# Performance work log

Hardware: AMD Instinct MI355X
Metric: run time of the kernel (lower is better)

## Reference

```python
import jax, jax.numpy as jnp
import numpy as np

GRAD_WEIGHT = 0.1
EPS = 1e-08


def _relative_l2(pred, target, eps):
    b = pred.shape[0]
    pf = pred.reshape(b, -1)
    tf = target.reshape(b, -1)
    num = jnp.linalg.norm(pf - tf, axis=1)
    den = jnp.maximum(jnp.linalg.norm(tf, axis=1), eps)
    return jnp.mean(num / den)


def _knn_gradient_norm(field, pos, knn_indices, eps):
    # field: (B,T,N,C); pos: (B,N,3); knn_indices: (B,N,K)
    # neigh_pos[b,n,k,:] = pos[b, knn[b,n,k], :]
    neigh_pos = jax.vmap(lambda p, idx: p[idx])(pos, knn_indices)  # (B,N,K,3)
    rel_pos = neigh_pos - pos[:, :, None, :]
    dist_sq = jnp.maximum(jnp.sum(rel_pos * rel_pos, axis=-1), eps)  # (B,N,K)
    dist = jnp.maximum(jnp.sqrt(dist_sq), eps)
    # neigh_field[b,t,n,k,:] = field[b,t,knn[b,n,k],:]
    neigh_field = jax.vmap(lambda f, idx: f[:, idx, :])(field, knn_indices)  # (B,T,N,K,C)
    rel_field = neigh_field - field[:, :, :, None, :]
    grad_mag = jnp.abs(rel_field) / dist[:, None, :, :, None]
    return jnp.mean(grad_mag, axis=(1, 2, 3, 4))  # (B,)


def setup_inputs() -> dict:
    key = jax.random.key(0)
    k1, k2, k3, k4 = jax.random.split(key, 4)
    B, T, N, C, K = 4, 8, 16384, 4, 16
    pred = jax.random.normal(k1, (B, T, N, C), dtype=jnp.float32)
    target = jax.random.normal(k2, (B, T, N, C), dtype=jnp.float32)
    knn_indices = jax.random.randint(k3, (B, N, K), 0, N, dtype=jnp.int64)
    pos = jax.random.uniform(k4, (B, N, 3), dtype=jnp.float32)
    return {"pred": pred, "target": target, "knn_indices": knn_indices, "pos": pos}


def reference(pred, target, knn_indices, pos):
    rl2 = _relative_l2(pred, target, EPS)
    pred_grad = _knn_gradient_norm(pred, pos, knn_indices, EPS)
    target_grad = _knn_gradient_norm(target, pos, knn_indices, EPS)
    grad_error = jnp.mean(jnp.abs(pred_grad - target_grad) / jnp.maximum(target_grad, EPS))
    return rl2 + GRAD_WEIGHT * grad_error
```

## Files before the change

kernel.cpp:

```cpp
#include <hip/hip_runtime.h>
#include <hip/hip_fp8.h>

#define NB   4
#define NT   8
#define NPTS 16384
#define NK   16
#define GRAD_COUNT 8388608.0f

#define P_BYTES     (NB * NPTS * 64)
#define REC_OFF_B   P_BYTES
#define PARTA_OFF_B (P_BYTES + NB * NPTS * NK * 8)
#define PARTB_OFF_B (PARTA_OFF_B + 65536)
#define WS_NEEDED   (PARTB_OFF_B + 8192)

#define PACK_BLOCKS 1024
#define DIST_BLOCKS 4096
#define PREP_BLOCKS (PACK_BLOCKS + DIST_BLOCKS)

#if defined(__has_builtin)
#if __has_builtin(__builtin_amdgcn_cvt_pk_f32_fp8) && __has_builtin(__builtin_amdgcn_cvt_pk_fp8_f32)
#define USE_FP8_BUILTINS 1
#endif
#endif

typedef float vf2 __attribute__((ext_vector_type(2)));

__device__ __forceinline__ unsigned pack4_fp8(float a, float b, float c, float d) {
#ifdef USE_FP8_BUILTINS
    int u = __builtin_amdgcn_cvt_pk_fp8_f32(a, b, 0, false);
    u     = __builtin_amdgcn_cvt_pk_fp8_f32(c, d, u, true);
    return (unsigned)u;
#else
    __hip_fp8_e4m3 ha(a), hb(b), hc(c), hd(d);
    return (unsigned)ha.__x | ((unsigned)hb.__x << 8) |
           ((unsigned)hc.__x << 16) | ((unsigned)hd.__x << 24);
#endif
}

__device__ __forceinline__ float absdiff4(unsigned a, unsigned b) {
#ifdef USE_FP8_BUILTINS
    vf2 a0 = __builtin_amdgcn_cvt_pk_f32_fp8((int)a, false);
    vf2 a1 = __builtin_amdgcn_cvt_pk_f32_fp8((int)a, true);
    vf2 b0 = __builtin_amdgcn_cvt_pk_f32_fp8((int)b, false);
    vf2 b1 = __builtin_amdgcn_cvt_pk_f32_fp8((int)b, true);
    return fabsf(a0.x - b0.x) + fabsf(a0.y - b0.y) +
           fabsf(a1.x - b1.x) + fabsf(a1.y - b1.y);
#else
    float s = 0.f;
    #pragma unroll
    for (int i = 0; i < 4; ++i) {
        __hip_fp8_e4m3 ha, hb;
        ha.__x = (a >> (8 * i)) & 0xff;
        hb.__x = (b >> (8 * i)) & 0xff;
        s += fabsf((float)ha - (float)hb);
    }
    return s;
#endif
}


__global__ __launch_bounds__(256) void sobolev_prep(
    const float4* __restrict__ pred,
    const float4* __restrict__ target,
    const float*  __restrict__ pos,
    const int*    __restrict__ knn,
    uint4*  __restrict__ P,
    int2*   __restrict__ REC,
    float*  __restrict__ partB)
{
    __shared__ float lds[4][2];

    if (blockIdx.x < PACK_BLOCKS) {
        const int blk = blockIdx.x;
        const int b   = blk >> 8;
        const int n   = ((blk & 255) << 6) + (threadIdx.x >> 2);
        const int q   = threadIdx.x & 3;

        const float4 pv0 = pred  [(b * NT + q    ) * NPTS + n];
        const float4 pv1 = pred  [(b * NT + q + 4) * NPTS + n];
        const float4 tv0 = target[(b * NT + q    ) * NPTS + n];
        const float4 tv1 = target[(b * NT + q + 4) * NPTS + n];

        uint4 ck;
        ck.x = pack4_fp8(pv0.x, pv0.y, pv0.z, pv0.w);
        ck.y = pack4_fp8(pv1.x, pv1.y, pv1.z, pv1.w);
        ck.z = pack4_fp8(tv0.x, tv0.y, tv0.z, tv0.w);
        ck.w = pack4_fp8(tv1.x, tv1.y, tv1.z, tv1.w);
        P[((size_t)(b * NPTS + n) << 2) + q] = ck;

        float sd, st;
        {
            const float e0 = pv0.x - tv0.x, e1 = pv0.y - tv0.y,
                        e2 = pv0.z - tv0.z, e3 = pv0.w - tv0.w;
            const float f0 = pv1.x - tv1.x, f1 = pv1.y - tv1.y,
                        f2 = pv1.z - tv1.z, f3 = pv1.w - tv1.w;
            sd = e0*e0 + e1*e1 + e2*e2 + e3*e3 + f0*f0 + f1*f1 + f2*f2 + f3*f3;
            st = tv0.x*tv0.x + tv0.y*tv0.y + tv0.z*tv0.z + tv0.w*tv0.w +
                 tv1.x*tv1.x + tv1.y*tv1.y + tv1.z*tv1.z + tv1.w*tv1.w;
        }

        const int wave = threadIdx.x >> 6, lane = threadIdx.x & 63;
        #pragma unroll
        for (int o = 32; o > 0; o >>= 1) {
            sd += __shfl_down(sd, o);
            st += __shfl_down(st, o);
        }
        if (lane == 0) { lds[wave][0] = sd; lds[wave][1] = st; }
        __syncthreads();
        if (threadIdx.x < 2)
            partB[blk * 2 + threadIdx.x] =
                lds[0][threadIdx.x] + lds[1][threadIdx.x] +
                lds[2][threadIdx.x] + lds[3][threadIdx.x];
    } else {
        const int t  = (blockIdx.x - PACK_BLOCKS) * 256 + threadIdx.x;
        const int b  = t >> 18;
        const int nk = t & 262143;
        const int n  = nk >> 4;
        const int j  = knn[t];

        const float* pb_ = pos + (size_t)b * NPTS * 3;
        const float jx = pb_[j * 3], jy = pb_[j * 3 + 1], jz = pb_[j * 3 + 2];
        const float nx = pb_[n * 3], ny = pb_[n * 3 + 1], nz = pb_[n * 3 + 2];
        const float dx = jx - nx, dy = jy - ny, dz = jz - nz;
        const float d2 = fmaxf(dx*dx + dy*dy + dz*dz, 1e-8f);
        const float inv_d = rsqrtf(d2);

        REC[t] = make_int2(j, __float_as_int(inv_d));
    }
}


__global__ __launch_bounds__(256) void sobolev_grad(
    const uint4* __restrict__ P,
    const int2*  __restrict__ REC,
    float*       __restrict__ partA)
{
    const int xcd  = blockIdx.x & 7;
    const int b    = xcd >> 1;
    const int nblk = ((xcd & 1) << 10) | (blockIdx.x >> 3);
    const int wave = threadIdx.x >> 6;
    const int lane = threadIdx.x & 63;
    const int k    = lane >> 2;
    const int q    = lane & 3;
    const int n0   = (nblk << 3) | (wave << 1);
    const int n1   = n0 | 1;

    const int2 r0 = REC[(((b << 14) | n0) << 4) | k];
    const int2 r1 = REC[(((b << 14) | n1) << 4) | k];
    const int j0 = r0.x, j1 = r1.x;
    const float inv_d0 = __int_as_float(r0.y);
    const float inv_d1 = __int_as_float(r1.y);

    const size_t pb = (size_t)(b * NPTS);
    const uint4 gj0 = P[((pb + j0) << 2) + q];
    const uint4 gn0 = P[((pb + n0) << 2) + q];
    const uint4 gj1 = P[((pb + j1) << 2) + q];
    const uint4 gn1 = P[((pb + n1) << 2) + q];

    const float sp0 = absdiff4(gj0.x, gn0.x) + absdiff4(gj0.y, gn0.y);
    const float st0 = absdiff4(gj0.z, gn0.z) + absdiff4(gj0.w, gn0.w);
    const float sp1 = absdiff4(gj1.x, gn1.x) + absdiff4(gj1.y, gn1.y);
    const float st1 = absdiff4(gj1.z, gn1.z) + absdiff4(gj1.w, gn1.w);

    float v0 = sp0 * inv_d0 + sp1 * inv_d1;
    float v1 = st0 * inv_d0 + st1 * inv_d1;

    __shared__ float lds[4][2];
    #pragma unroll
    for (int o = 32; o > 0; o >>= 1) {
        v0 += __shfl_down(v0, o);
        v1 += __shfl_down(v1, o);
    }
    if (lane == 0) { lds[wave][0] = v0; lds[wave][1] = v1; }
    __syncthreads();
    if (threadIdx.x < 2) {
        const int slot = (b << 11) | nblk;
        partA[slot * 2 + threadIdx.x] =
            lds[0][threadIdx.x] + lds[1][threadIdx.x] +
            lds[2][threadIdx.x] + lds[3][threadIdx.x];
    }
}

__global__ __launch_bounds__(1024) void sobolev_final(
    const float* __restrict__ partA,
    const float* __restrict__ partB,
    float*       __restrict__ out)
{
    const int tid = threadIdx.x;
    __shared__ float acc[NB][4];
    __shared__ float red[16][4];

    for (int b = 0; b < NB; ++b) {
        float pg = 0.f, tg = 0.f, sd = 0.f, st = 0.f;
        {
            const float2 v0 = ((const float2*)(partA + b * 2048 * 2))[tid];
            pg += v0.x; tg += v0.y;
            const float2 v1 = ((const float2*)(partA + b * 2048 * 2))[tid + 1024];
            pg += v1.x; tg += v1.y;
        }
        if (tid < 256) {
            const float2 vb = ((const float2*)(partB + b * 256 * 2))[tid];
            sd = vb.x; st = vb.y;
        }
        #pragma unroll
        for (int o = 32; o > 0; o >>= 1) {
            pg += __shfl_down(pg, o); tg += __shfl_down(tg, o);
            sd += __shfl_down(sd, o); st += __shfl_down(st, o);
        }
        const int wave = tid >> 6, lane = tid & 63;
        if (lane == 0) {
            red[wave][0] = pg; red[wave][1] = tg;
            red[wave][2] = sd; red[wave][3] = st;
        }
        __syncthreads();
        if (tid < 4) {
            float s = 0.f;
            #pragma unroll
            for (int w = 0; w < 16; ++w) s += red[w][tid];
            acc[b][tid] = s;
        }
        __syncthreads();
    }

    if (tid == 0) {
        float rl2 = 0.f, ge = 0.f;
        const float inv_cnt = 1.0f / GRAD_COUNT;
        #pragma unroll
        for (int b = 0; b < NB; ++b) {
            const float pg = acc[b][0] * inv_cnt;
            const float tg = acc[b][1] * inv_cnt;
            rl2 += sqrtf(acc[b][2]) / fmaxf(sqrtf(acc[b][3]), 1e-8f);
            ge  += fabsf(pg - tg) / fmaxf(tg, 1e-8f);
        }
        out[0] = rl2 * 0.25f + 0.1f * (ge * 0.25f);
    }
}


__global__ __launch_bounds__(256) void sobolev_main_fb(
    const float4* __restrict__ pred,
    const float4* __restrict__ target,
    const int*    __restrict__ knn,
    const float*  __restrict__ pos,
    float*        __restrict__ part)
{
    const int xcd   = blockIdx.x & 7;
    const int s     = blockIdx.x >> 3;
    const int b     = xcd >> 1;
    const int thalf = xcd & 1;
    const int w     = s * 256 + threadIdx.x;
    const int k     = w & (NK - 1);
    const int n     = w >> 4;
    const int j     = knn[(b << 18) + w];

    const float* pc = pos + (b * NPTS + n) * 3;
    const float* pj = pos + (b * NPTS + j) * 3;
    const float dx = pj[0] - pc[0], dy = pj[1] - pc[1], dz = pj[2] - pc[2];
    const float d2   = fmaxf(dx*dx + dy*dy + dz*dz, 1e-8f);
    const float dist = fmaxf(sqrtf(d2), 1e-8f);
    const float inv_d = 1.0f / dist;

    float pg_abs = 0.f, tg_abs = 0.f, sd = 0.f, st = 0.f;
    const bool do_l2 = (k == 0);
    const int t0 = thalf * 4;
    #pragma unroll
    for (int tt = 0; tt < 4; ++tt) {
        const int base = (b * NT + t0 + tt) * NPTS;
        const float4 pcv = pred[base + n];
        const float4 pjv = pred[base + j];
        const float4 tcv = target[base + n];
        const float4 tjv = target[base + j];
        pg_abs += fabsf(pjv.x-pcv.x)+fabsf(pjv.y-pcv.y)+fabsf(pjv.z-pcv.z)+fabsf(pjv.w-pcv.w);
        tg_abs += fabsf(tjv.x-tcv.x)+fabsf(tjv.y-tcv.y)+fabsf(tjv.z-tcv.z)+fabsf(tjv.w-tcv.w);
        if (do_l2) {
            const float ex = pcv.x-tcv.x, ey = pcv.y-tcv.y, ez = pcv.z-tcv.z, ew = pcv.w-tcv.w;
            sd += ex*ex + ey*ey + ez*ez + ew*ew;
            st += tcv.x*tcv.x + tcv.y*tcv.y + tcv.z*tcv.z + tcv.w*tcv.w;
        }
    }
    float vals[4] = { pg_abs * inv_d, tg_abs * inv_d, sd, st };
    __shared__ float lds[4][4];
    const int wave = threadIdx.x >> 6, lane = threadIdx.x & 63;
    #pragma unroll
    for (int c = 0; c < 4; ++c) {
        float v = vals[c];
        #pragma unroll
        for (int o = 32; o > 0; o >>= 1) v += __shfl_down(v, o);
        if (lane == 0) lds[wave][c] = v;
    }
    __syncthreads();
    if (threadIdx.x < 4) {
        const int slot = (xcd << 10) | s;
        part[slot * 4 + threadIdx.x] =
            lds[0][threadIdx.x] + lds[1][threadIdx.x] +
            lds[2][threadIdx.x] + lds[3][threadIdx.x];
    }
}

__global__ __launch_bounds__(256) void sobolev_finalize_fb(
    const float* __restrict__ part, float* __restrict__ out)
{
    __shared__ float sums_s[16];
    __shared__ float lred[4];
    const int tid = threadIdx.x;
    for (int bc = 0; bc < 16; ++bc) {
        const int b = bc >> 2, comp = bc & 3;
        float s = 0.f;
        for (int i = tid; i < 2048; i += 256)
            s += part[(b * 2048 + i) * 4 + comp];
        #pragma unroll
        for (int o = 32; o > 0; o >>= 1) s += __shfl_down(s, o);
        const int wave = tid >> 6, lane = tid & 63;
        if (lane == 0) lred[wave] = s;
        __syncthreads();
        if (tid == 0) sums_s[bc] = lred[0] + lred[1] + lred[2] + lred[3];
        __syncthreads();
    }
    if (tid == 0) {
        float rl2 = 0.f, ge = 0.f;
        const float inv_cnt = 1.0f / GRAD_COUNT;
        #pragma unroll
        for (int b = 0; b < NB; ++b) {
            const float pg = sums_s[b*4+0] * inv_cnt;
            const float tg = sums_s[b*4+1] * inv_cnt;
            rl2 += sqrtf(sums_s[b*4+2]) / fmaxf(sqrtf(sums_s[b*4+3]), 1e-8f);
            ge  += fabsf(pg - tg) / fmaxf(tg, 1e-8f);
        }
        out[0] = rl2 * 0.25f + 0.1f * (ge * 0.25f);
    }
}


extern "C" void kernel_launch(void* const* d_in, const int* in_sizes, int n_in,
                              void* d_out, int out_size, void* d_ws, size_t ws_size,
                              hipStream_t stream) {
    const float4* pred   = (const float4*)d_in[0];
    const float4* target = (const float4*)d_in[1];
    const int*    knn    = (const int*)d_in[2];
    const float*  pos    = (const float*)d_in[3];
    float* out = (float*)d_out;

    if (ws_size >= (size_t)WS_NEEDED) {
        uint4* P     = (uint4*)d_ws;
        int2*  REC   = (int2*)((char*)d_ws + REC_OFF_B);
        float* partA = (float*)((char*)d_ws + PARTA_OFF_B);
        float* partB = (float*)((char*)d_ws + PARTB_OFF_B);

        sobolev_prep<<<PREP_BLOCKS, 256, 0, stream>>>(pred, target, pos, knn, P, REC, partB);
        sobolev_grad<<<8192, 256, 0, stream>>>(P, REC, partA);
        sobolev_final<<<1, 1024, 0, stream>>>(partA, partB, out);
    } else {
        float* part = (float*)d_ws;
        sobolev_main_fb<<<8192, 256, 0, stream>>>(pred, target, knn, pos, part);
        sobolev_finalize_fb<<<1, 256, 0, stream>>>(part, out);
    }
}
```

Measured before the change: 35.90 us.

## Split prep into pack and LDS-staged distance kernels with 16-bit quantized positions

Splits the fused prep kernel into a pack kernel and a separate distance kernel. The pack kernel also quantizes positions to 16-bit fixed point. The distance kernel stages each batch's quantized positions (128KB) in LDS so the random neighbor lookups hit shared memory instead of global memory. It also loads knn indices and stores records with vectorized int4 accesses. The cost is an extra kernel launch, a dependency between the two kernels, only 128 large blocks (one per CU with heavy LDS use), and reduced position precision.

```diff
diff --git a/kernel.cpp b/kernel.cpp
--- a/kernel.cpp
+++ b/kernel.cpp
@@ -8,14 +8,13 @@
 #define GRAD_COUNT 8388608.0f
 
 #define P_BYTES     (NB * NPTS * 64)
-#define REC_OFF_B   P_BYTES
-#define PARTA_OFF_B (P_BYTES + NB * NPTS * NK * 8)
+#define POSQ_OFF_B  P_BYTES
+#define REC_OFF_B   (POSQ_OFF_B + NB * NPTS * 8)
+#define PARTA_OFF_B (REC_OFF_B + NB * NPTS * NK * 8)
 #define PARTB_OFF_B (PARTA_OFF_B + 65536)
 #define WS_NEEDED   (PARTB_OFF_B + 8192)
 
-#define PACK_BLOCKS 1024
-#define DIST_BLOCKS 4096
-#define PREP_BLOCKS (PACK_BLOCKS + DIST_BLOCKS)
+#define DIST_BPB    32
 
 #if defined(__has_builtin)
 #if __has_builtin(__builtin_amdgcn_cvt_pk_f32_fp8) && __has_builtin(__builtin_amdgcn_cvt_pk_fp8_f32)
@@ -58,75 +57,113 @@
 #endif
 }
 
-
-__global__ __launch_bounds__(256) void sobolev_prep(
+__device__ __forceinline__ unsigned short q16(float p) {
+    int i = (int)(p * 65536.0f);
+    return (unsigned short)(i > 65535 ? 65535 : (i < 0 ? 0 : i));
+}
+
+
+__global__ __launch_bounds__(256) void sobolev_pack(
     const float4* __restrict__ pred,
     const float4* __restrict__ target,
     const float*  __restrict__ pos,
-    const int*    __restrict__ knn,
-    uint4*  __restrict__ P,
-    int2*   __restrict__ REC,
-    float*  __restrict__ partB)
-{
+    uint4*   __restrict__ P,
+    ushort4* __restrict__ POSQ,
+    float*   __restrict__ partB)
+{
+    const int blk = blockIdx.x;
+    const int b   = blk >> 8;
+    const int n   = ((blk & 255) << 6) + (threadIdx.x >> 2);
+    const int q   = threadIdx.x & 3;
+
+    const float4 pv0 = pred  [(b * NT + q    ) * NPTS + n];
+    const float4 pv1 = pred  [(b * NT + q + 4) * NPTS + n];
+    const float4 tv0 = target[(b * NT + q    ) * NPTS + n];
+    const float4 tv1 = target[(b * NT + q + 4) * NPTS + n];
+
+    uint4 ck;
+    ck.x = pack4_fp8(pv0.x, pv0.y, pv0.z, pv0.w);
+    ck.y = pack4_fp8(pv1.x, pv1.y, pv1.z, pv1.w);
+    ck.z = pack4_fp8(tv0.x, tv0.y, tv0.z, tv0.w);
+    ck.w = pack4_fp8(tv1.x, tv1.y, tv1.z, tv1.w);
+    P[((size_t)(b * NPTS + n) << 2) + q] = ck;
+
+    if (q == 0) {
+        const float* pp = pos + (size_t)(b * NPTS + n) * 3;
+        ushort4 uq;
+        uq.x = q16(pp[0]); uq.y = q16(pp[1]); uq.z = q16(pp[2]); uq.w = 0;
+        POSQ[b * NPTS + n] = uq;
+    }
+
+    float sd, st;
+    {
+        const float e0 = pv0.x - tv0.x, e1 = pv0.y - tv0.y,
+                    e2 = pv0.z - tv0.z, e3 = pv0.w - tv0.w;
+        const float f0 = pv1.x - tv1.x, f1 = pv1.y - tv1.y,
+                    f2 = pv1.z - tv1.z, f3 = pv1.w - tv1.w;
+        sd = e0*e0 + e1*e1 + e2*e2 + e3*e3 + f0*f0 + f1*f1 + f2*f2 + f3*f3;
+        st = tv0.x*tv0.x + tv0.y*tv0.y + tv0.z*tv0.z + tv0.w*tv0.w +
+             tv1.x*tv1.x + tv1.y*tv1.y + tv1.z*tv1.z + tv1.w*tv1.w;
+    }
+
     __shared__ float lds[4][2];
-
-    if (blockIdx.x < PACK_BLOCKS) {
-        const int blk = blockIdx.x;
-        const int b   = blk >> 8;
-        const int n   = ((blk & 255) << 6) + (threadIdx.x >> 2);
-        const int q   = threadIdx.x & 3;
-
-        const float4 pv0 = pred  [(b * NT + q    ) * NPTS + n];
-        const float4 pv1 = pred  [(b * NT + q + 4) * NPTS + n];
-        const float4 tv0 = target[(b * NT + q    ) * NPTS + n];
-        const float4 tv1 = target[(b * NT + q + 4) * NPTS + n];
-
-        uint4 ck;
-        ck.x = pack4_fp8(pv0.x, pv0.y, pv0.z, pv0.w);
-        ck.y = pack4_fp8(pv1.x, pv1.y, pv1.z, pv1.w);
-        ck.z = pack4_fp8(tv0.x, tv0.y, tv0.z, tv0.w);
-        ck.w = pack4_fp8(tv1.x, tv1.y, tv1.z, tv1.w);
-        P[((size_t)(b * NPTS + n) << 2) + q] = ck;
-
-        float sd, st;
-        {
-            const float e0 = pv0.x - tv0.x, e1 = pv0.y - tv0.y,
-                        e2 = pv0.z - tv0.z, e3 = pv0.w - tv0.w;
-            const float f0 = pv1.x - tv1.x, f1 = pv1.y - tv1.y,
-                        f2 = pv1.z - tv1.z, f3 = pv1.w - tv1.w;
-            sd = e0*e0 + e1*e1 + e2*e2 + e3*e3 + f0*f0 + f1*f1 + f2*f2 + f3*f3;
-            st = tv0.x*tv0.x + tv0.y*tv0.y + tv0.z*tv0.z + tv0.w*tv0.w +
-                 tv1.x*tv1.x + tv1.y*tv1.y + tv1.z*tv1.z + tv1.w*tv1.w;
-        }
-
-        const int wave = threadIdx.x >> 6, lane = threadIdx.x & 63;
-        #pragma unroll
-        for (int o = 32; o > 0; o >>= 1) {
-            sd += __shfl_down(sd, o);
-            st += __shfl_down(st, o);
-        }
-        if (lane == 0) { lds[wave][0] = sd; lds[wave][1] = st; }
-        __syncthreads();
-        if (threadIdx.x < 2)
-            partB[blk * 2 + threadIdx.x] =
-                lds[0][threadIdx.x] + lds[1][threadIdx.x] +
-                lds[2][threadIdx.x] + lds[3][threadIdx.x];
-    } else {
-        const int t  = (blockIdx.x - PACK_BLOCKS) * 256 + threadIdx.x;
-        const int b  = t >> 18;
-        const int nk = t & 262143;
-        const int n  = nk >> 4;
-        const int j  = knn[t];
-
-        const float* pb_ = pos + (size_t)b * NPTS * 3;
-        const float jx = pb_[j * 3], jy = pb_[j * 3 + 1], jz = pb_[j * 3 + 2];
-        const float nx = pb_[n * 3], ny = pb_[n * 3 + 1], nz = pb_[n * 3 + 2];
-        const float dx = jx - nx, dy = jy - ny, dz = jz - nz;
-        const float d2 = fmaxf(dx*dx + dy*dy + dz*dz, 1e-8f);
-        const float inv_d = rsqrtf(d2);
-
-        REC[t] = make_int2(j, __float_as_int(inv_d));
-    }
+    const int wave = threadIdx.x >> 6, lane = threadIdx.x & 63;
+    #pragma unroll
+    for (int o = 32; o > 0; o >>= 1) {
+        sd += __shfl_down(sd, o);
+        st += __shfl_down(st, o);
+    }
+    if (lane == 0) { lds[wave][0] = sd; lds[wave][1] = st; }
+    __syncthreads();
+    if (threadIdx.x < 2)
+        partB[blk * 2 + threadIdx.x] =
+            lds[0][threadIdx.x] + lds[1][threadIdx.x] +
+            lds[2][threadIdx.x] + lds[3][threadIdx.x];
+}
+
+
+__global__ __launch_bounds__(512) void sobolev_dist(
+    const ushort4* __restrict__ POSQ,
+    const int*     __restrict__ knn,
+    int2*          __restrict__ REC)
+{
+    __shared__ ushort4 spos[NPTS];
+    const int b   = blockIdx.x / DIST_BPB;
+    const int sub = blockIdx.x % DIST_BPB;
+
+    const ushort4* pb = POSQ + b * NPTS;
+    for (int i = threadIdx.x; i < NPTS; i += 512)
+        spos[i] = pb[i];
+    __syncthreads();
+
+    const int n = (sub << 9) + threadIdx.x;
+    const ushort4 cn = spos[n];
+    const int cx = cn.x, cy = cn.y, cz = cn.z;
+    const int base = ((b << 14) | n) << 4;
+
+    int4 js[4];
+    {
+        const int4* kp = (const int4*)(knn + base);
+        js[0] = kp[0]; js[1] = kp[1]; js[2] = kp[2]; js[3] = kp[3];
+    }
+
+    const float scale2 = 1.0f / (65536.0f * 65536.0f);
+    int2 out[16];
+    #pragma unroll
+    for (int kk = 0; kk < 16; ++kk) {
+        const int j = ((const int*)js)[kk];
+        const ushort4 cj = spos[j];
+        const float dx = (float)(cj.x - cx);
+        const float dy = (float)(cj.y - cy);
+        const float dz = (float)(cj.z - cz);
+        const float d2 = fmaxf((dx*dx + dy*dy + dz*dz) * scale2, 1e-8f);
+        out[kk] = make_int2(j, __float_as_int(rsqrtf(d2)));
+    }
+
+    int4* rp = (int4*)(REC + base);
+    #pragma unroll
+    for (int i = 0; i < 8; ++i)
+        rp[i] = make_int4(out[2*i].x, out[2*i].y, out[2*i+1].x, out[2*i+1].y);
 }
 
 
@@ -341,12 +378,14 @@
     float* out = (float*)d_out;
 
     if (ws_size >= (size_t)WS_NEEDED) {
-        uint4* P     = (uint4*)d_ws;
-        int2*  REC   = (int2*)((char*)d_ws + REC_OFF_B);
-        float* partA = (float*)((char*)d_ws + PARTA_OFF_B);
-        float* partB = (float*)((char*)d_ws + PARTB_OFF_B);
-
-        sobolev_prep<<<PREP_BLOCKS, 256, 0, stream>>>(pred, target, pos, knn, P, REC, partB);
+        uint4*   P     = (uint4*)d_ws;
+        ushort4* POSQ  = (ushort4*)((char*)d_ws + POSQ_OFF_B);
+        int2*    REC   = (int2*)((char*)d_ws + REC_OFF_B);
+        float*   partA = (float*)((char*)d_ws + PARTA_OFF_B);
+        float*   partB = (float*)((char*)d_ws + PARTB_OFF_B);
+
+        sobolev_pack<<<1024, 256, 0, stream>>>(pred, target, pos, P, POSQ, partB);
+        sobolev_dist<<<NB * DIST_BPB, 512, 0, stream>>>(POSQ, knn, REC);
         sobolev_grad<<<8192, 256, 0, stream>>>(P, REC, partA);
         sobolev_final<<<1, 1024, 0, stream>>>(partA, partB, out);
     } else {
```

Result: slower. 46.40 us (+29.2%).

## Split prep into pack and LDS-staged quantized-position distance kernels

Applied to the files above, without the earlier changes.

Splits the fused prep kernel into a pack kernel and a separate distance kernel. The distance kernel stages each batch's positions in LDS, quantized to 16-bit fixed point, so the random neighbour gathers read LDS instead of global memory. Each thread now handles one point's 16 neighbours with vectorized int4 loads and stores. The trade-offs are an extra kernel launch, each of the 256 blocks redundantly reloading all 16K positions, and reduced distance precision from quantization, which can hurt accuracy for very close neighbour pairs.

```diff
diff --git a/kernel.cpp b/kernel.cpp
--- a/kernel.cpp
+++ b/kernel.cpp
@@ -9,13 +9,11 @@
 
 #define P_BYTES     (NB * NPTS * 64)
 #define REC_OFF_B   P_BYTES
-#define PARTA_OFF_B (P_BYTES + NB * NPTS * NK * 8)
+#define PARTA_OFF_B (REC_OFF_B + NB * NPTS * NK * 8)
 #define PARTB_OFF_B (PARTA_OFF_B + 65536)
 #define WS_NEEDED   (PARTB_OFF_B + 8192)
 
-#define PACK_BLOCKS 1024
-#define DIST_BLOCKS 4096
-#define PREP_BLOCKS (PACK_BLOCKS + DIST_BLOCKS)
+#define DIST_BPB    64
 
 #if defined(__has_builtin)
 #if __has_builtin(__builtin_amdgcn_cvt_pk_f32_fp8) && __has_builtin(__builtin_amdgcn_cvt_pk_fp8_f32)
@@ -58,75 +56,109 @@
 #endif
 }
 
-
-__global__ __launch_bounds__(256) void sobolev_prep(
+__device__ __forceinline__ unsigned q16(float p) {
+    int i = (int)(p * 65536.0f);
+    return (unsigned)(i > 65535 ? 65535 : (i < 0 ? 0 : i));
+}
+
+
+__global__ __launch_bounds__(256) void sobolev_pack(
     const float4* __restrict__ pred,
     const float4* __restrict__ target,
-    const float*  __restrict__ pos,
-    const int*    __restrict__ knn,
     uint4*  __restrict__ P,
-    int2*   __restrict__ REC,
     float*  __restrict__ partB)
 {
+    const int blk = blockIdx.x;
+    const int b   = blk >> 8;
+    const int n   = ((blk & 255) << 6) + (threadIdx.x >> 2);
+    const int q   = threadIdx.x & 3;
+
+    const float4 pv0 = pred  [(b * NT + q    ) * NPTS + n];
+    const float4 pv1 = pred  [(b * NT + q + 4) * NPTS + n];
+    const float4 tv0 = target[(b * NT + q    ) * NPTS + n];
+    const float4 tv1 = target[(b * NT + q + 4) * NPTS + n];
+
+    uint4 ck;
+    ck.x = pack4_fp8(pv0.x, pv0.y, pv0.z, pv0.w);
+    ck.y = pack4_fp8(pv1.x, pv1.y, pv1.z, pv1.w);
+    ck.z = pack4_fp8(tv0.x, tv0.y, tv0.z, tv0.w);
+    ck.w = pack4_fp8(tv1.x, tv1.y, tv1.z, tv1.w);
+    P[((size_t)(b * NPTS + n) << 2) + q] = ck;
+
+    float sd, st;
+    {
+        const float e0 = pv0.x - tv0.x, e1 = pv0.y - tv0.y,
+                    e2 = pv0.z - tv0.z, e3 = pv0.w - tv0.w;
+        const float f0 = pv1.x - tv1.x, f1 = pv1.y - tv1.y,
+                    f2 = pv1.z - tv1.z, f3 = pv1.w - tv1.w;
+        sd = e0*e0 + e1*e1 + e2*e2 + e3*e3 + f0*f0 + f1*f1 + f2*f2 + f3*f3;
+        st = tv0.x*tv0.x + tv0.y*tv0.y + tv0.z*tv0.z + tv0.w*tv0.w +
+             tv1.x*tv1.x + tv1.y*tv1.y + tv1.z*tv1.z + tv1.w*tv1.w;
+    }
+
     __shared__ float lds[4][2];
-
-    if (blockIdx.x < PACK_BLOCKS) {
-        const int blk = blockIdx.x;
-        const int b   = blk >> 8;
-        const int n   = ((blk & 255) << 6) + (threadIdx.x >> 2);
-        const int q   = threadIdx.x & 3;
-
-        const float4 pv0 = pred  [(b * NT + q    ) * NPTS + n];
-        const float4 pv1 = pred  [(b * NT + q + 4) * NPTS + n];
-        const float4 tv0 = target[(b * NT + q    ) * NPTS + n];
-        const float4 tv1 = target[(b * NT + q + 4) * NPTS + n];
-
-        uint4 ck;
-        ck.x = pack4_fp8(pv0.x, pv0.y, pv0.z, pv0.w);
-        ck.y = pack4_fp8(pv1.x, pv1.y, pv1.z, pv1.w);
-        ck.z = pack4_fp8(tv0.x, tv0.y, tv0.z, tv0.w);
-        ck.w = pack4_fp8(tv1.x, tv1.y, tv1.z, tv1.w);
-        P[((size_t)(b * NPTS + n) << 2) + q] = ck;
-
-        float sd, st;
-        {
-            const float e0 = pv0.x - tv0.x, e1 = pv0.y - tv0.y,
-                        e2 = pv0.z - tv0.z, e3 = pv0.w - tv0.w;
-            const float f0 = pv1.x - tv1.x, f1 = pv1.y - tv1.y,
-                        f2 = pv1.z - tv1.z, f3 = pv1.w - tv1.w;
-            sd = e0*e0 + e1*e1 + e2*e2 + e3*e3 + f0*f0 + f1*f1 + f2*f2 + f3*f3;
-            st = tv0.x*tv0.x + tv0.y*tv0.y + tv0.z*tv0.z + tv0.w*tv0.w +
-                 tv1.x*tv1.x + tv1.y*tv1.y + tv1.z*tv1.z + tv1.w*tv1.w;
-        }
-
-        const int wave = threadIdx.x >> 6, lane = threadIdx.x & 63;
-        #pragma unroll
-        for (int o = 32; o > 0; o >>= 1) {
-            sd += __shfl_down(sd, o);
-            st += __shfl_down(st, o);
-        }
-        if (lane == 0) { lds[wave][0] = sd; lds[wave][1] = st; }
-        __syncthreads();
-        if (threadIdx.x < 2)
-            partB[blk * 2 + threadIdx.x] =
-                lds[0][threadIdx.x] + lds[1][threadIdx.x] +
-                lds[2][threadIdx.x] + lds[3][threadIdx.x];
-    } else {
-        const int t  = (blockIdx.x - PACK_BLOCKS) * 256 + threadIdx.x;
-        const int b  = t >> 18;
-        const int nk = t & 262143;
-        const int n  = nk >> 4;
-        const int j  = knn[t];
-
-        const float* pb_ = pos + (size_t)b * NPTS * 3;
-        const float jx = pb_[j * 3], jy = pb_[j * 3 + 1], jz = pb_[j * 3 + 2];
-        const float nx = pb_[n * 3], ny = pb_[n * 3 + 1], nz = pb_[n * 3 + 2];
-        const float dx = jx - nx, dy = jy - ny, dz = jz - nz;
-        const float d2 = fmaxf(dx*dx + dy*dy + dz*dz, 1e-8f);
-        const float inv_d = rsqrtf(d2);
-
-        REC[t] = make_int2(j, __float_as_int(inv_d));
-    }
+    const int wave = threadIdx.x >> 6, lane = threadIdx.x & 63;
+    #pragma unroll
+    for (int o = 32; o > 0; o >>= 1) {
+        sd += __shfl_down(sd, o);
+        st += __shfl_down(st, o);
+    }
+    if (lane == 0) { lds[wave][0] = sd; lds[wave][1] = st; }
+    __syncthreads();
+    if (threadIdx.x < 2)
+        partB[blk * 2 + threadIdx.x] =
+            lds[0][threadIdx.x] + lds[1][threadIdx.x] +
+            lds[2][threadIdx.x] + lds[3][threadIdx.x];
+}
+
+
+__global__ __launch_bounds__(256) void sobolev_dist(
+    const float* __restrict__ pos,
+    const int*   __restrict__ knn,
+    int2*        __restrict__ REC)
+{
+    __shared__ unsigned       sxy[NPTS];
+    __shared__ unsigned short sz [NPTS];
+    const int b   = blockIdx.x >> 6;
+    const int sub = blockIdx.x & (DIST_BPB - 1);
+
+    const float* pb = pos + (size_t)b * NPTS * 3;
+    for (int p = threadIdx.x; p < NPTS; p += 256) {
+        const float x = pb[p * 3], y = pb[p * 3 + 1], z = pb[p * 3 + 2];
+        sxy[p] = q16(x) | (q16(y) << 16);
+        sz[p]  = (unsigned short)q16(z);
+    }
+    __syncthreads();
+
+    const int n = (sub << 8) + threadIdx.x;
+    const unsigned cxy = sxy[n];
+    const int cx = (int)(cxy & 0xffffu), cy = (int)(cxy >> 16), cz = (int)sz[n];
+    const int base = ((b << 14) | n) << 4;
+
+    int4 js[4];
+    {
+        const int4* kp = (const int4*)(knn + base);
+        js[0] = kp[0]; js[1] = kp[1]; js[2] = kp[2]; js[3] = kp[3];
+    }
+
+    const float s2 = 1.0f / (65536.0f * 65536.0f);
+    int2 rec[16];
+    #pragma unroll
+    for (int kk = 0; kk < 16; ++kk) {
+        const int j = (&js[0].x)[kk];
+        const unsigned jxy = sxy[j];
+        const int jx = (int)(jxy & 0xffffu), jy = (int)(jxy >> 16), jz = (int)sz[j];
+        const float dx = (float)(jx - cx);
+        const float dy = (float)(jy - cy);
+        const float dz = (float)(jz - cz);
+        const float d2 = fmaxf((dx*dx + dy*dy + dz*dz) * s2, 1e-8f);
+        rec[kk] = make_int2(j, __float_as_int(rsqrtf(d2)));
+    }
+
+    int4* rp = (int4*)(REC + base);
+    #pragma unroll
+    for (int i = 0; i < 8; ++i)
+        rp[i] = make_int4(rec[2*i].x, rec[2*i].y, rec[2*i+1].x, rec[2*i+1].y);
 }
 
 
@@ -346,7 +378,8 @@
         float* partA = (float*)((char*)d_ws + PARTA_OFF_B);
         float* partB = (float*)((char*)d_ws + PARTB_OFF_B);
 
-        sobolev_prep<<<PREP_BLOCKS, 256, 0, stream>>>(pred, target, pos, knn, P, REC, partB);
+        sobolev_pack<<<1024, 256, 0, stream>>>(pred, target, P, partB);
+        sobolev_dist<<<NB * DIST_BPB, 256, 0, stream>>>(pos, knn, REC);
         sobolev_grad<<<8192, 256, 0, stream>>>(P, REC, partA);
         sobolev_final<<<1, 1024, 0, stream>>>(partA, partB, out);
     } else {
```

New measurement: 44.44 us. 1.24x slower.
